# Performance work log

Measured on AMD Instinct MI355X. Metric: run time of the kernel, lower is better.

Reference implementation:

```python
import jax, jax.numpy as jnp
import numpy as np

WINDOWS = ((0, 4), (2, 6), (4, 8))
N_CLASSES = 64
EPS = 1e-12  # F.normalize eps


def setup_inputs() -> dict:
    key = jax.random.key(0)
    k1, k2 = jax.random.split(key)
    S, Q, T, D = 256, 4096, 8, 1024
    support_features = jax.random.normal(k1, (S, T, D), dtype=jnp.float32)
    target_features = jax.random.normal(k2, (Q, T, D), dtype=jnp.float32)
    support_labels = jnp.arange(S, dtype=jnp.int32) % N_CLASSES  # 4 shots per class, sorted-unique order
    logit_scale = jnp.array(0.0, dtype=jnp.float32)
    fusion_logits = jnp.zeros((3,), dtype=jnp.float32)
    return {
        'support_features': support_features,
        'target_features': target_features,
        'support_labels': support_labels,
        'logit_scale': logit_scale,
        'fusion_logits': fusion_logits,
    }


def _l2norm(x):
    n = jnp.sqrt(jnp.sum(x * x, axis=-1, keepdims=True))
    return x / jnp.maximum(n, EPS)


def _pairwise_dist(query_seq, support_seq):
    # query_seq: [Q, Tq, D], support_seq: [K, Ts, D] -> 1 - cosine sim [Q, K, Tq, Ts]
    sim = jnp.einsum('qtd,ksd->qkts', _l2norm(query_seq), _l2norm(support_seq))
    return 1.0 - sim


def _bi_mhm(dists):
    # dists: [Q, K, Tq, Ts]
    return dists.min(axis=3).sum(axis=2) + dists.min(axis=2).sum(axis=2)


def _segments(features):
    # features: [N, T, D] -> [N, n_windows, D] (mean over each window)
    return jnp.stack([features[:, s:e, :].mean(axis=1) for s, e in WINDOWS], axis=1)


def _prototypes(features, labels):
    # scatter-mean over class labels; features: [S, ...], labels: [S]
    sums = jax.ops.segment_sum(features, labels, num_segments=N_CLASSES)
    counts = jax.ops.segment_sum(jnp.ones((features.shape[0],), features.dtype), labels,
                                 num_segments=N_CLASSES)
    return sums / counts[:, None, None]


def reference(support_features, target_features, support_labels, logit_scale, fusion_logits):
    # global (frame-level) bidirectional min-sum chamfer distance to class prototypes
    support_proto = _prototypes(support_features, support_labels)          # [K, T, D]
    global_dist = _bi_mhm(_pairwise_dist(target_features, support_proto))  # [Q, K]

    # segment-level distances
    support_segments = _segments(support_features)                          # [S, 3, D]
    target_segments = _segments(target_features)                            # [Q, 3, D]
    support_seg_proto = _prototypes(support_segments, support_labels)       # [K, 3, D]
    seg_dist = _pairwise_dist(target_segments, support_seg_proto)           # [Q, K, 3, 3]
    seg_q2s = seg_dist.min(axis=3).sum(axis=2)
    seg_s2q = seg_dist.min(axis=2).sum(axis=2)

    fusion = jax.nn.softmax(fusion_logits)
    fused = (fusion[0] * global_dist + fusion[1] * seg_s2q + fusion[2] * seg_q2s)
    fused = fused * jnp.exp(logit_scale)
    return (-fused, -global_dist, -seg_s2q, -seg_q2s)
```

## Files before the change

### kernel.cpp

```cpp
#include <hip/hip_runtime.h>
#include <stdint.h>

typedef unsigned short u16;
typedef short short8 __attribute__((ext_vector_type(8)));
typedef float floatx4 __attribute__((ext_vector_type(4)));

#define KDIM 1024
#define QN   4096
#define KCLS 64
#define QK   (QN * KCLS)

#define DPP_XOR1 0xB1
#define DPP_XOR2 0x4E
#define DPP_HMIR 0x141
#define SWZ_XOR6  0x181F
#define SWZ_XOR16 0x401F

template <int CTRL>
__device__ __forceinline__ float dppf(float x) {
  int r = __builtin_amdgcn_mov_dpp(__builtin_bit_cast(int, x), CTRL, 0xF, 0xF, true);
  return __builtin_bit_cast(float, r);
}
template <int OFF>
__device__ __forceinline__ float swzf(float x) {
  int r = __builtin_amdgcn_ds_swizzle(__builtin_bit_cast(int, x), OFF);
  return __builtin_bit_cast(float, r);
}
__device__ __forceinline__ float max8(float x) {
  x = fmaxf(x, dppf<DPP_XOR1>(x));
  x = fmaxf(x, dppf<DPP_XOR2>(x));
  x = fmaxf(x, dppf<DPP_HMIR>(x));
  return x;
}
__device__ __forceinline__ float sum8(float x) {
  x += dppf<DPP_XOR1>(x);
  x += dppf<DPP_XOR2>(x);
  x += dppf<DPP_HMIR>(x);
  return x;
}


__device__ __forceinline__ u16 f2bf(float x) {
  union { float f; uint32_t u; } un; un.f = x;
  uint32_t u = un.u;
  u += 0x7FFFu + ((u >> 16) & 1u);
  return (u16)(u >> 16);
}

struct alignas(16) F4 { float x, y, z, w; };
struct alignas(8)  U16x4 { u16 a, b, c, d; };

__device__ __forceinline__ float dot4(const F4& a, const F4& b) {
  return a.x*b.x + a.y*b.y + a.z*b.z + a.w*b.w;
}

__device__ __forceinline__ void reduce11(float (&ss)[11], float (&tot)[11],
                                         float (*sb)[12], int lane, int wave) {
  #pragma unroll
  for (int v = 0; v < 11; ++v) {
    float x = ss[v];
    #pragma unroll
    for (int m = 1; m < 64; m <<= 1) x += __shfl_xor(x, m);
    ss[v] = x;
  }
  if (lane == 0) {
    #pragma unroll
    for (int v = 0; v < 11; ++v) sb[wave][v] = ss[v];
  }
  __syncthreads();
  #pragma unroll
  for (int v = 0; v < 11; ++v)
    tot[v] = sb[0][v] + sb[1][v] + sb[2][v] + sb[3][v];
}

__device__ __forceinline__ float inv_norm(float ss) {
  return 1.0f / fmaxf(sqrtf(ss), 1e-12f);
}

__global__ __launch_bounds__(256) void prep_all(const float* __restrict__ T,
                                                const float* __restrict__ S,
                                                u16* __restrict__ Ag,
                                                u16* __restrict__ Bg,
                                                float* __restrict__ invnT,
                                                float* __restrict__ invnTw,
                                                float* __restrict__ invnS,
                                                float* __restrict__ invnSw) {
  __shared__ float sb[4][12];
  const int b = blockIdx.x, tid = threadIdx.x;
  const int lane = tid & 63, wave = tid >> 6;

  if (b < QN) {
    const int q = b;
    F4 x[8];
    #pragma unroll
    for (int t = 0; t < 8; ++t)
      x[t] = *(const F4*)(T + (size_t)(q*8 + t)*1024 + tid*4);

    float ss[11], tot[11];
    #pragma unroll
    for (int t = 0; t < 8; ++t) ss[t] = dot4(x[t], x[t]);
    #pragma unroll
    for (int w = 0; w < 3; ++w) {
      F4 y;
      y.x = (x[2*w].x + x[2*w+1].x + x[2*w+2].x + x[2*w+3].x) * 0.25f;
      y.y = (x[2*w].y + x[2*w+1].y + x[2*w+2].y + x[2*w+3].y) * 0.25f;
      y.z = (x[2*w].z + x[2*w+1].z + x[2*w+2].z + x[2*w+3].z) * 0.25f;
      y.w = (x[2*w].w + x[2*w+1].w + x[2*w+2].w + x[2*w+3].w) * 0.25f;
      ss[8+w] = dot4(y, y);
    }
    reduce11(ss, tot, sb, lane, wave);

    #pragma unroll
    for (int t = 0; t < 8; ++t) {
      U16x4 o; o.a = f2bf(x[t].x); o.b = f2bf(x[t].y);
      o.c = f2bf(x[t].z); o.d = f2bf(x[t].w);
      *(U16x4*)(Ag + (size_t)(q*8 + t)*1024 + tid*4) = o;
    }
    if (tid < 8)       invnT [q*8 + tid]     = inv_norm(tot[tid]);
    else if (tid < 11) invnTw[q*4 + tid - 8] = inv_norm(tot[tid]);
  } else {
    const int k = b - QN;
    F4 p[8];
    #pragma unroll
    for (int t = 0; t < 8; ++t) { p[t].x = 0.f; p[t].y = 0.f; p[t].z = 0.f; p[t].w = 0.f; }
    #pragma unroll
    for (int s = 0; s < 4; ++s)
      #pragma unroll
      for (int t = 0; t < 8; ++t) {
        const F4 v = *(const F4*)(S + (size_t)(((s*64 + k)*8 + t))*1024 + tid*4);
        p[t].x += v.x; p[t].y += v.y; p[t].z += v.z; p[t].w += v.w;
      }
    float ss[11], tot[11];
    #pragma unroll
    for (int t = 0; t < 8; ++t) ss[t] = dot4(p[t], p[t]) * 0.0625f;
    #pragma unroll
    for (int w = 0; w < 3; ++w) {
      F4 y;
      y.x = (p[2*w].x + p[2*w+1].x + p[2*w+2].x + p[2*w+3].x) * 0.0625f;
      y.y = (p[2*w].y + p[2*w+1].y + p[2*w+2].y + p[2*w+3].y) * 0.0625f;
      y.z = (p[2*w].z + p[2*w+1].z + p[2*w+2].z + p[2*w+3].z) * 0.0625f;
      y.w = (p[2*w].w + p[2*w+1].w + p[2*w+2].w + p[2*w+3].w) * 0.0625f;
      ss[8+w] = dot4(y, y);
    }
    reduce11(ss, tot, sb, lane, wave);

    #pragma unroll
    for (int t = 0; t < 8; ++t) {
      U16x4 o; o.a = f2bf(p[t].x*0.25f); o.b = f2bf(p[t].y*0.25f);
      o.c = f2bf(p[t].z*0.25f); o.d = f2bf(p[t].w*0.25f);
      *(U16x4*)(Bg + (size_t)(k*8 + t)*1024 + tid*4) = o;
    }
    if (tid < 8)       invnS [k*8 + tid]     = inv_norm(tot[tid]);
    else if (tid < 11) invnSw[k*4 + tid - 8] = inv_norm(tot[tid]) * 0.0625f;
  }
}


__device__ __forceinline__ void load_lds16(const u16* g, u16* l) {
  __builtin_amdgcn_global_load_lds((__attribute__((address_space(1))) void*)(g),
                                   (__attribute__((address_space(3))) void*)(l),
                                   16, 0, 0);
}

__global__ __launch_bounds__(256) void gemm_all(const u16* __restrict__ A,
                                                const u16* __restrict__ B,
                                                const float* __restrict__ invnT,
                                                const float* __restrict__ invnTw,
                                                const float* __restrict__ invnS,
                                                const float* __restrict__ invnSw,
                                                float* __restrict__ outF,
                                                float* __restrict__ outG,
                                                float* __restrict__ outS2Q,
                                                float* __restrict__ outQ2S,
                                                const float* __restrict__ fl,
                                                const float* __restrict__ ls) {
  __shared__ __align__(16) u16 At[128 * 128];
  __shared__ __align__(16) u16 Bt[128 * 128];

  const int tid  = threadIdx.x;
  const int lane = tid & 63;
  const int wave = tid >> 6;
  const int wm = wave >> 1, wn = wave & 1;
  const int rowA0 = blockIdx.x * 128;
  const int rowB0 = blockIdx.y * 128;

  floatx4 acc[4][4] = {};

  const int srow = lane >> 4;
  const int sl   = lane & 15;

  for (int kb = 0; kb < KDIM; kb += 128) {
    __syncthreads();
    #pragma unroll
    for (int it = 0; it < 8; ++it) {
      const int c   = wave * 8 + it;
      const int row = c * 4 + srow;
      const int scol = ((sl ^ (row & 7)) * 8);
      load_lds16(A + (size_t)(rowA0 + row) * KDIM + kb + scol, &At[c * 512]);
      load_lds16(B + (size_t)(rowB0 + row) * KDIM + kb + scol, &Bt[c * 512]);
    }
    __syncthreads();
    const int q4 = lane >> 4;
    #pragma unroll
    for (int kk = 0; kk < 4; ++kk) {
      const int kc0 = kk * 4 + q4;
      short8 af[4], bf[4];
      #pragma unroll
      for (int i = 0; i < 4; ++i) {
        const int row = wm*64 + i*16 + (lane & 15);
        af[i] = *(const short8*)&At[row*128 + ((kc0 ^ (row & 7)) * 8)];
        const int col = wn*64 + i*16 + (lane & 15);
        bf[i] = *(const short8*)&Bt[col*128 + ((kc0 ^ (col & 7)) * 8)];
      }
      #pragma unroll
      for (int i = 0; i < 4; ++i)
        #pragma unroll
        for (int j = 0; j < 4; ++j)
          acc[i][j] = __builtin_amdgcn_mfma_f32_16x16x32_bf16(af[i], bf[j], acc[i][j], 0, 0, 0);
    }
  }

  const int sIdx = lane & 7;
  const int b3 = (lane >> 3) & 1;
  const int b4 = (lane >> 4) & 1;
  const int b5 = lane >> 5;
  const int qL = blockIdx.x * 16 + wm * 8;
  const int kL = blockIdx.y * 16 + wn * 8;

  float invT[4][4], invTw3[4][3], invS[4], invSw3[4][3];
  #pragma unroll
  for (int i = 0; i < 4; ++i) {
    const int q = qL + i*2 + b5;
    #pragma unroll
    for (int r = 0; r < 4; ++r) invT[i][r] = invnT[q*8 + b4*4 + r];
    #pragma unroll
    for (int w = 0; w < 3; ++w) invTw3[i][w] = invnTw[q*4 + w];
  }
  #pragma unroll
  for (int j = 0; j < 4; ++j) {
    const int k = kL + j*2 + b3;
    invS[j] = invnS[k*8 + sIdx];
    #pragma unroll
    for (int v = 0; v < 3; ++v) invSw3[j][v] = invnSw[k*4 + v];
  }

  const float f0 = fl[0], f1 = fl[1], f2 = fl[2];
  const float mx = fmaxf(f0, fmaxf(f1, f2));
  const float e0 = __expf(f0 - mx), e1 = __expf(f1 - mx), e2 = __expf(f2 - mx);
  const float sc = __expf(ls[0]) / (e0 + e1 + e2);

  const int vA = (sIdx < 4) ? 0 : 2;
  const bool v1ok = (sIdx >= 2) && (sIdx <= 5);

  #pragma unroll
  for (int i = 0; i < 4; ++i) {
    #pragma unroll
    for (int j = 0; j < 4; ++j) {
      const floatx4 c = acc[i][j];

      float sim[4];
      #pragma unroll
      for (int r = 0; r < 4; ++r) sim[r] = c[r] * invT[i][r] * invS[j];
      float rs = 0.f;
      #pragma unroll
      for (int r = 0; r < 4; ++r) rs += max8(sim[r]);
      rs += swzf<SWZ_XOR16>(rs);
      float cm = fmaxf(fmaxf(sim[0], sim[1]), fmaxf(sim[2], sim[3]));
      cm = fmaxf(cm, swzf<SWZ_XOR16>(cm));
      const float cs = sum8(cm);
      const float g = rs + cs - 16.0f;

      float wA[4], wB[4];
      #pragma unroll
      for (int r = 0; r < 4; ++r) {
        const float p2 = c[r] + dppf<DPP_XOR1>(c[r]);
        wA[r] = p2 + dppf<DPP_XOR2>(p2);
        wB[r] = p2 + swzf<SWZ_XOR6>(p2);
      }
      float twA[3], twB[3];
      {
        const float aAll = wA[0] + wA[1] + wA[2] + wA[3];
        const float aOth = swzf<SWZ_XOR16>(aAll);
        twA[0] = b4 ? aOth : aAll;
        twA[2] = b4 ? aAll : aOth;
        const float aH = b4 ? (wA[0] + wA[1]) : (wA[2] + wA[3]);
        twA[1] = aH + swzf<SWZ_XOR16>(aH);
        const float bAll = wB[0] + wB[1] + wB[2] + wB[3];
        const float bOth = swzf<SWZ_XOR16>(bAll);
        twB[0] = b4 ? bOth : bAll;
        twB[2] = b4 ? bAll : bOth;
        const float bH = b4 ? (wB[0] + wB[1]) : (wB[2] + wB[3]);
        twB[1] = bH + swzf<SWZ_XOR16>(bH);
      }
      float pA[3], pB[3];
      #pragma unroll
      for (int w = 0; w < 3; ++w) {
        pA[w] = twA[w] * invTw3[i][w] * invSw3[j][vA];
        pB[w] = twB[w] * invTw3[i][w] * invSw3[j][1];
      }
      float q2s = 0.f;
      #pragma unroll
      for (int w = 0; w < 3; ++w)
        q2s += max8(v1ok ? fmaxf(pA[w], pB[w]) : pA[w]);
      const float mwA = fmaxf(fmaxf(pA[0], pA[1]), pA[2]);
      const float mwB = fmaxf(fmaxf(pB[0], pB[1]), pB[2]);
      float contrib = ((sIdx == 0) | (sIdx == 4)) ? mwA : 0.f;
      if (sIdx == 2) contrib += mwB;
      const float s2q = sum8(contrib);

      if ((lane & 23) == 0) {
        const int q = qL + i*2 + b5;
        const int k = kL + j*2 + b3;
        const size_t idx = (size_t)q * KCLS + k;
        const float o1 = g;
        const float o2 = s2q - 3.0f;
        const float o3 = q2s - 3.0f;
        outG[idx]   = o1;
        outS2Q[idx] = o2;
        outQ2S[idx] = o3;
        outF[idx]   = sc * (e0 * o1 + e1 * o2 + e2 * o3);
      }
    }
  }
}


extern "C" void kernel_launch(void* const* d_in, const int* in_sizes, int n_in,
                              void* d_out, int out_size, void* d_ws, size_t ws_size,
                              hipStream_t stream) {
  (void)in_sizes; (void)n_in; (void)out_size; (void)ws_size;
  const float* S  = (const float*)d_in[0];
  const float* T  = (const float*)d_in[1];
  const float* ls = (const float*)d_in[3];
  const float* fl = (const float*)d_in[4];

  float* outF   = (float*)d_out;
  float* outG   = outF + QK;
  float* outS2Q = outF + 2 * (size_t)QK;
  float* outQ2S = outF + 3 * (size_t)QK;

  u16*   Ag     = (u16*)d_ws;
  u16*   Bg     = Ag + (size_t)32768 * 1024;
  float* invnT  = (float*)(Bg + (size_t)512 * 1024);
  float* invnTw = invnT + 32768;
  float* invnS  = invnTw + 16384;
  float* invnSw = invnS + 512;

  prep_all<<<QN + KCLS, 256, 0, stream>>>(T, S, Ag, Bg, invnT, invnTw, invnS, invnSw);

  gemm_all<<<dim3(256, 4), 256, 0, stream>>>(Ag, Bg, invnT, invnTw, invnS, invnSw,
                                             outF, outG, outS2Q, outQ2S, fl, ls);
}
```

Before: 268.3 us.

## Rewrite GEMM as 256x256 tile with double-buffered pipelined LDS staging

```diff
diff --git a/kernel.cpp b/kernel.cpp
--- a/kernel.cpp
+++ b/kernel.cpp
@@ -9,6 +9,7 @@
 #define QN   4096
 #define KCLS 64
 #define QK   (QN * KCLS)
+#define NKT  16
 
 #define DPP_XOR1 0xB1
 #define DPP_XOR2 0x4E
@@ -162,74 +163,160 @@
                                    16, 0, 0);
 }
 
-__global__ __launch_bounds__(256) void gemm_all(const u16* __restrict__ A,
-                                                const u16* __restrict__ B,
-                                                const float* __restrict__ invnT,
-                                                const float* __restrict__ invnTw,
-                                                const float* __restrict__ invnS,
-                                                const float* __restrict__ invnSw,
-                                                float* __restrict__ outF,
-                                                float* __restrict__ outG,
-                                                float* __restrict__ outS2Q,
-                                                float* __restrict__ outQ2S,
-                                                const float* __restrict__ fl,
-                                                const float* __restrict__ ls) {
-  __shared__ __align__(16) u16 At[128 * 128];
-  __shared__ __align__(16) u16 Bt[128 * 128];
+__device__ __forceinline__ void stage_half(const u16* __restrict__ A,
+                                           const u16* __restrict__ B,
+                                           u16* At_, u16* Bt_, int h,
+                                           int rowA0, int rowB0, int wave, int lane) {
+  const int tau = h >> 2, eta = h & 3;
+  const int kb = tau * 64;
+  const int half = eta & 1;
+  const int srow = lane >> 3, sl = lane & 7;
+  const int scol = (sl ^ srow) * 8;
+  const int region = (tau & 1) * 2 + half;
+  const int gr0 = ((eta < 2) ? rowA0 : rowB0) + half * 128;
+  const u16* gsrc = (eta < 2) ? A : B;
+  u16* ldst = (eta < 2) ? At_ : Bt_;
+  #pragma unroll
+  for (int r = 0; r < 2; ++r) {
+    const int c = r * 8 + wave;
+    const int row = c * 8 + srow;
+    load_lds16(gsrc + (size_t)(gr0 + row) * KDIM + kb + scol,
+               ldst + region * 8192 + c * 512);
+  }
+}
+
+__device__ __forceinline__ void ld_a(short8 (&dst)[4][2], const u16* At_,
+                                     int region, int lane, int i0) {
+  const int m = lane & 15, g = lane >> 4, r7 = lane & 7;
+  const u16* base = At_ + region * 8192;
+  #pragma unroll
+  for (int i = 0; i < 4; ++i)
+    #pragma unroll
+    for (int s = 0; s < 2; ++s) {
+      const int kc = s * 4 + g;
+      dst[i][s] = *(const short8*)&base[(i0 + i) * 1024 + m * 64 + ((kc ^ r7) * 8)];
+    }
+}
+
+__device__ __forceinline__ void ld_b(short8 (&dst)[2][2], const u16* Bt_,
+                                     int region, int colb, int lane, int j0) {
+  const int m = lane & 15, g = lane >> 4, r7 = lane & 7;
+  const u16* base = Bt_ + region * 8192;
+  #pragma unroll
+  for (int j = 0; j < 2; ++j)
+    #pragma unroll
+    for (int s = 0; s < 2; ++s) {
+      const int kc = s * 4 + g;
+      dst[j][s] = *(const short8*)&base[(colb + (j0 + j) * 16 + m) * 64 + ((kc ^ r7) * 8)];
+    }
+}
+
+#define SB()    __builtin_amdgcn_s_barrier()
+#define SCHED() __builtin_amdgcn_sched_barrier(0)
+#define MFMA16(AF, BF, I0, J0)                                                  \
+  do {                                                                          \
+    __builtin_amdgcn_s_setprio(1);                                              \
+    _Pragma("unroll") for (int i_ = 0; i_ < 4; ++i_)                            \
+      _Pragma("unroll") for (int j_ = 0; j_ < 2; ++j_)                          \
+        _Pragma("unroll") for (int s_ = 0; s_ < 2; ++s_)                        \
+          acc[(I0)+i_][(J0)+j_] = __builtin_amdgcn_mfma_f32_16x16x32_bf16(      \
+              AF[i_][s_], BF[j_][s_], acc[(I0)+i_][(J0)+j_], 0, 0, 0);          \
+    __builtin_amdgcn_s_setprio(0);                                              \
+  } while (0)
+
+__global__ __launch_bounds__(512, 2) void gemm_all(const u16* __restrict__ A,
+                                                   const u16* __restrict__ B,
+                                                   const float* __restrict__ invnT,
+                                                   const float* __restrict__ invnTw,
+                                                   const float* __restrict__ invnS,
+                                                   const float* __restrict__ invnSw,
+                                                   float* __restrict__ outF,
+                                                   float* __restrict__ outG,
+                                                   float* __restrict__ outS2Q,
+                                                   float* __restrict__ outQ2S,
+                                                   const float* __restrict__ fl,
+                                                   const float* __restrict__ ls) {
+  __shared__ __align__(16) u16 At[4 * 128 * 64];
+  __shared__ __align__(16) u16 Bt[4 * 128 * 64];
 
   const int tid  = threadIdx.x;
   const int lane = tid & 63;
   const int wave = tid >> 6;
-  const int wm = wave >> 1, wn = wave & 1;
-  const int rowA0 = blockIdx.x * 128;
-  const int rowB0 = blockIdx.y * 128;
-
-  floatx4 acc[4][4] = {};
-
-  const int srow = lane >> 4;
-  const int sl   = lane & 15;
-
-  for (int kb = 0; kb < KDIM; kb += 128) {
-    __syncthreads();
-    #pragma unroll
-    for (int it = 0; it < 8; ++it) {
-      const int c   = wave * 8 + it;
-      const int row = c * 4 + srow;
-      const int scol = ((sl ^ (row & 7)) * 8);
-      load_lds16(A + (size_t)(rowA0 + row) * KDIM + kb + scol, &At[c * 512]);
-      load_lds16(B + (size_t)(rowB0 + row) * KDIM + kb + scol, &Bt[c * 512]);
-    }
-    __syncthreads();
-    const int q4 = lane >> 4;
-    #pragma unroll
-    for (int kk = 0; kk < 4; ++kk) {
-      const int kc0 = kk * 4 + q4;
-      short8 af[4], bf[4];
-      #pragma unroll
-      for (int i = 0; i < 4; ++i) {
-        const int row = wm*64 + i*16 + (lane & 15);
-        af[i] = *(const short8*)&At[row*128 + ((kc0 ^ (row & 7)) * 8)];
-        const int col = wn*64 + i*16 + (lane & 15);
-        bf[i] = *(const short8*)&Bt[col*128 + ((kc0 ^ (col & 7)) * 8)];
-      }
-      #pragma unroll
-      for (int i = 0; i < 4; ++i)
-        #pragma unroll
-        for (int j = 0; j < 4; ++j)
-          acc[i][j] = __builtin_amdgcn_mfma_f32_16x16x32_bf16(af[i], bf[j], acc[i][j], 0, 0, 0);
-    }
+  const int wm = wave >> 2;
+  const int wn = wave & 3;
+  const int rowA0 = blockIdx.x * 256;
+  const int rowB0 = blockIdx.y * 256;
+  const int colb = (wn & 1) * 64;
+
+  floatx4 acc[8][4] = {};
+  short8 a0[4][2], a1[4][2], b0[2][2], b1[2][2];
+
+  #pragma unroll
+  for (int h = 0; h < 6; ++h)
+    stage_half(A, B, At, Bt, h, rowA0, rowB0, wave, lane);
+
+  #pragma unroll 1
+  for (int t = 0; t < NKT - 1; ++t) {
+    const int buf = t & 1;
+    const int ra = buf * 2 + wm;
+    const int rb = buf * 2 + (wn >> 1);
+    stage_half(A, B, At, Bt, 4*t + 6, rowA0, rowB0, wave, lane);
+    SCHED();
+    asm volatile("s_waitcnt vmcnt(6)");
+    SCHED();
+    SB(); SCHED();
+    ld_a(a0, At, ra, lane, 0);
+    ld_b(b0, Bt, rb, colb, lane, 0);
+    MFMA16(a0, b0, 0, 0);
+    SB(); SCHED();
+    stage_half(A, B, At, Bt, 4*t + 7, rowA0, rowB0, wave, lane);
+    SCHED();
+    SB(); SCHED();
+    ld_a(a1, At, ra, lane, 4);
+    MFMA16(a1, b0, 4, 0);
+    SB(); SCHED();
+    if (4*t + 8 < 4*NKT)
+      stage_half(A, B, At, Bt, 4*t + 8, rowA0, rowB0, wave, lane);
+    SCHED();
+    SB(); SCHED();
+    ld_b(b1, Bt, rb, colb, lane, 2);
+    MFMA16(a0, b1, 0, 2);
+    SB(); SCHED();
+    if (4*t + 9 < 4*NKT)
+      stage_half(A, B, At, Bt, 4*t + 9, rowA0, rowB0, wave, lane);
+    SCHED();
+    SB(); SCHED();
+    MFMA16(a1, b1, 4, 2);
+    SB(); SCHED();
+  }
+  {
+    const int ra = 2 + wm;
+    const int rb = 2 + (wn >> 1);
+    asm volatile("s_waitcnt vmcnt(0)");
+    SCHED();
+    SB(); SCHED();
+    ld_a(a0, At, ra, lane, 0);
+    ld_b(b0, Bt, rb, colb, lane, 0);
+    MFMA16(a0, b0, 0, 0);
+    SB(); SCHED();
+    ld_a(a1, At, ra, lane, 4);
+    MFMA16(a1, b0, 4, 0);
+    SB(); SCHED();
+    ld_b(b1, Bt, rb, colb, lane, 2);
+    MFMA16(a0, b1, 0, 2);
+    MFMA16(a1, b1, 4, 2);
   }
 
   const int sIdx = lane & 7;
   const int b3 = (lane >> 3) & 1;
   const int b4 = (lane >> 4) & 1;
   const int b5 = lane >> 5;
-  const int qL = blockIdx.x * 16 + wm * 8;
-  const int kL = blockIdx.y * 16 + wn * 8;
-
-  float invT[4][4], invTw3[4][3], invS[4], invSw3[4][3];
-  #pragma unroll
-  for (int i = 0; i < 4; ++i) {
+  const int qL = blockIdx.x * 32 + wm * 16;
+  const int kL = blockIdx.y * 32 + wn * 8;
+
+  float invT[8][4], invTw3[8][3], invS[4], invSw3[4][3];
+  #pragma unroll
+  for (int i = 0; i < 8; ++i) {
     const int q = qL + i*2 + b5;
     #pragma unroll
     for (int r = 0; r < 4; ++r) invT[i][r] = invnT[q*8 + b4*4 + r];
@@ -253,7 +340,7 @@
   const bool v1ok = (sIdx >= 2) && (sIdx <= 5);
 
   #pragma unroll
-  for (int i = 0; i < 4; ++i) {
+  for (int i = 0; i < 8; ++i) {
     #pragma unroll
     for (int j = 0; j < 4; ++j) {
       const floatx4 c = acc[i][j];
@@ -348,6 +435,6 @@
 
   prep_all<<<QN + KCLS, 256, 0, stream>>>(T, S, Ag, Bg, invnT, invnTw, invnS, invnSw);
 
-  gemm_all<<<dim3(256, 4), 256, 0, stream>>>(Ag, Bg, invnT, invnTw, invnS, invnSw,
+  gemm_all<<<dim3(128, 2), 512, 0, stream>>>(Ag, Bg, invnT, invnTw, invnS, invnSw,
                                              outF, outG, outS2Q, outQ2S, fl, ls);
 }
```

After: 266.0 us. No clear change (-0.8%).

## Fuse query bf16 conversion and norms into GEMM with double-buffered B staging

Applied to the files above, without the earlier changes.

```diff
diff --git a/kernel.cpp b/kernel.cpp
--- a/kernel.cpp
+++ b/kernel.cpp
@@ -9,6 +9,7 @@
 #define QN   4096
 #define KCLS 64
 #define QK   (QN * KCLS)
+#define NKT  16
 
 #define DPP_XOR1 0xB1
 #define DPP_XOR2 0x4E
@@ -54,107 +55,12 @@
   return a.x*b.x + a.y*b.y + a.z*b.z + a.w*b.w;
 }
 
-__device__ __forceinline__ void reduce11(float (&ss)[11], float (&tot)[11],
-                                         float (*sb)[12], int lane, int wave) {
-  #pragma unroll
-  for (int v = 0; v < 11; ++v) {
-    float x = ss[v];
-    #pragma unroll
-    for (int m = 1; m < 64; m <<= 1) x += __shfl_xor(x, m);
-    ss[v] = x;
-  }
-  if (lane == 0) {
-    #pragma unroll
-    for (int v = 0; v < 11; ++v) sb[wave][v] = ss[v];
-  }
-  __syncthreads();
-  #pragma unroll
-  for (int v = 0; v < 11; ++v)
-    tot[v] = sb[0][v] + sb[1][v] + sb[2][v] + sb[3][v];
-}
-
 __device__ __forceinline__ float inv_norm(float ss) {
   return 1.0f / fmaxf(sqrtf(ss), 1e-12f);
 }
 
-__global__ __launch_bounds__(256) void prep_all(const float* __restrict__ T,
-                                                const float* __restrict__ S,
-                                                u16* __restrict__ Ag,
-                                                u16* __restrict__ Bg,
-                                                float* __restrict__ invnT,
-                                                float* __restrict__ invnTw,
-                                                float* __restrict__ invnS,
-                                                float* __restrict__ invnSw) {
-  __shared__ float sb[4][12];
-  const int b = blockIdx.x, tid = threadIdx.x;
-  const int lane = tid & 63, wave = tid >> 6;
-
-  if (b < QN) {
-    const int q = b;
-    F4 x[8];
-    #pragma unroll
-    for (int t = 0; t < 8; ++t)
-      x[t] = *(const F4*)(T + (size_t)(q*8 + t)*1024 + tid*4);
-
-    float ss[11], tot[11];
-    #pragma unroll
-    for (int t = 0; t < 8; ++t) ss[t] = dot4(x[t], x[t]);
-    #pragma unroll
-    for (int w = 0; w < 3; ++w) {
-      F4 y;
-      y.x = (x[2*w].x + x[2*w+1].x + x[2*w+2].x + x[2*w+3].x) * 0.25f;
-      y.y = (x[2*w].y + x[2*w+1].y + x[2*w+2].y + x[2*w+3].y) * 0.25f;
-      y.z = (x[2*w].z + x[2*w+1].z + x[2*w+2].z + x[2*w+3].z) * 0.25f;
-      y.w = (x[2*w].w + x[2*w+1].w + x[2*w+2].w + x[2*w+3].w) * 0.25f;
-      ss[8+w] = dot4(y, y);
-    }
-    reduce11(ss, tot, sb, lane, wave);
-
-    #pragma unroll
-    for (int t = 0; t < 8; ++t) {
-      U16x4 o; o.a = f2bf(x[t].x); o.b = f2bf(x[t].y);
-      o.c = f2bf(x[t].z); o.d = f2bf(x[t].w);
-      *(U16x4*)(Ag + (size_t)(q*8 + t)*1024 + tid*4) = o;
-    }
-    if (tid < 8)       invnT [q*8 + tid]     = inv_norm(tot[tid]);
-    else if (tid < 11) invnTw[q*4 + tid - 8] = inv_norm(tot[tid]);
-  } else {
-    const int k = b - QN;
-    F4 p[8];
-    #pragma unroll
-    for (int t = 0; t < 8; ++t) { p[t].x = 0.f; p[t].y = 0.f; p[t].z = 0.f; p[t].w = 0.f; }
-    #pragma unroll
-    for (int s = 0; s < 4; ++s)
-      #pragma unroll
-      for (int t = 0; t < 8; ++t) {
-        const F4 v = *(const F4*)(S + (size_t)(((s*64 + k)*8 + t))*1024 + tid*4);
-        p[t].x += v.x; p[t].y += v.y; p[t].z += v.z; p[t].w += v.w;
-      }
-    float ss[11], tot[11];
-    #pragma unroll
-    for (int t = 0; t < 8; ++t) ss[t] = dot4(p[t], p[t]) * 0.0625f;
-    #pragma unroll
-    for (int w = 0; w < 3; ++w) {
-      F4 y;
-      y.x = (p[2*w].x + p[2*w+1].x + p[2*w+2].x + p[2*w+3].x) * 0.0625f;
-      y.y = (p[2*w].y + p[2*w+1].y + p[2*w+2].y + p[2*w+3].y) * 0.0625f;
-      y.z = (p[2*w].z + p[2*w+1].z + p[2*w+2].z + p[2*w+3].z) * 0.0625f;
-      y.w = (p[2*w].w + p[2*w+1].w + p[2*w+2].w + p[2*w+3].w) * 0.0625f;
-      ss[8+w] = dot4(y, y);
-    }
-    reduce11(ss, tot, sb, lane, wave);
-
-    #pragma unroll
-    for (int t = 0; t < 8; ++t) {
-      U16x4 o; o.a = f2bf(p[t].x*0.25f); o.b = f2bf(p[t].y*0.25f);
-      o.c = f2bf(p[t].z*0.25f); o.d = f2bf(p[t].w*0.25f);
-      *(U16x4*)(Bg + (size_t)(k*8 + t)*1024 + tid*4) = o;
-    }
-    if (tid < 8)       invnS [k*8 + tid]     = inv_norm(tot[tid]);
-    else if (tid < 11) invnSw[k*4 + tid - 8] = inv_norm(tot[tid]) * 0.0625f;
-  }
-}
-
+#define SB()    __builtin_amdgcn_s_barrier()
+#define SCHED() __builtin_amdgcn_sched_barrier(0)
 
 __device__ __forceinline__ void load_lds16(const u16* g, u16* l) {
   __builtin_amdgcn_global_load_lds((__attribute__((address_space(1))) void*)(g),
@@ -162,86 +68,220 @@
                                    16, 0, 0);
 }
 
-__global__ __launch_bounds__(256) void gemm_all(const u16* __restrict__ A,
-                                                const u16* __restrict__ B,
-                                                const float* __restrict__ invnT,
-                                                const float* __restrict__ invnTw,
-                                                const float* __restrict__ invnS,
-                                                const float* __restrict__ invnSw,
-                                                float* __restrict__ outF,
-                                                float* __restrict__ outG,
-                                                float* __restrict__ outS2Q,
-                                                float* __restrict__ outQ2S,
-                                                const float* __restrict__ fl,
-                                                const float* __restrict__ ls) {
-  __shared__ __align__(16) u16 At[128 * 128];
-  __shared__ __align__(16) u16 Bt[128 * 128];
+__global__ __launch_bounds__(256) void prep_B(const float* __restrict__ S,
+                                              u16* __restrict__ Bg,
+                                              float* __restrict__ invnS,
+                                              float* __restrict__ invnSw) {
+  __shared__ float sb[4][12];
+  const int k = blockIdx.x, tid = threadIdx.x;
+  const int lane = tid & 63, wave = tid >> 6;
+
+  F4 p[8];
+  #pragma unroll
+  for (int t = 0; t < 8; ++t) { p[t].x = 0.f; p[t].y = 0.f; p[t].z = 0.f; p[t].w = 0.f; }
+  #pragma unroll
+  for (int s = 0; s < 4; ++s)
+    #pragma unroll
+    for (int t = 0; t < 8; ++t) {
+      const F4 v = *(const F4*)(S + (size_t)(((s*64 + k)*8 + t))*1024 + tid*4);
+      p[t].x += v.x; p[t].y += v.y; p[t].z += v.z; p[t].w += v.w;
+    }
+  float ss[11], tot[11];
+  #pragma unroll
+  for (int t = 0; t < 8; ++t) ss[t] = dot4(p[t], p[t]) * 0.0625f;
+  #pragma unroll
+  for (int w = 0; w < 3; ++w) {
+    F4 y;
+    y.x = (p[2*w].x + p[2*w+1].x + p[2*w+2].x + p[2*w+3].x) * 0.0625f;
+    y.y = (p[2*w].y + p[2*w+1].y + p[2*w+2].y + p[2*w+3].y) * 0.0625f;
+    y.z = (p[2*w].z + p[2*w+1].z + p[2*w+2].z + p[2*w+3].z) * 0.0625f;
+    y.w = (p[2*w].w + p[2*w+1].w + p[2*w+2].w + p[2*w+3].w) * 0.0625f;
+    ss[8+w] = dot4(y, y);
+  }
+  #pragma unroll
+  for (int v = 0; v < 11; ++v) {
+    float x = ss[v];
+    #pragma unroll
+    for (int m = 1; m < 64; m <<= 1) x += __shfl_xor(x, m);
+    ss[v] = x;
+  }
+  if (lane == 0) {
+    #pragma unroll
+    for (int v = 0; v < 11; ++v) sb[wave][v] = ss[v];
+  }
+  __syncthreads();
+  #pragma unroll
+  for (int v = 0; v < 11; ++v)
+    tot[v] = sb[0][v] + sb[1][v] + sb[2][v] + sb[3][v];
+
+  #pragma unroll
+  for (int t = 0; t < 8; ++t) {
+    U16x4 o; o.a = f2bf(p[t].x*0.25f); o.b = f2bf(p[t].y*0.25f);
+    o.c = f2bf(p[t].z*0.25f); o.d = f2bf(p[t].w*0.25f);
+    *(U16x4*)(Bg + (size_t)(k*8 + t)*1024 + tid*4) = o;
+  }
+  if (tid < 8)       invnS [k*8 + tid]     = inv_norm(tot[tid]);
+  else if (tid < 11) invnSw[k*4 + tid - 8] = inv_norm(tot[tid]) * 0.0625f;
+}
+
+__global__ __launch_bounds__(512, 1) void fused_all(const float* __restrict__ T,
+                                                    const u16* __restrict__ Bg,
+                                                    const float* __restrict__ invnS,
+                                                    const float* __restrict__ invnSw,
+                                                    float* __restrict__ outF,
+                                                    float* __restrict__ outG,
+                                                    float* __restrict__ outS2Q,
+                                                    float* __restrict__ outQ2S,
+                                                    const float* __restrict__ fl,
+                                                    const float* __restrict__ ls) {
+  __shared__ __align__(16) u16 At[128 * 64];
+  __shared__ __align__(16) u16 Bt[2][512 * 64];
 
   const int tid  = threadIdx.x;
   const int lane = tid & 63;
   const int wave = tid >> 6;
-  const int wm = wave >> 1, wn = wave & 1;
-  const int rowA0 = blockIdx.x * 128;
-  const int rowB0 = blockIdx.y * 128;
-
-  floatx4 acc[4][4] = {};
-
-  const int srow = lane >> 4;
-  const int sl   = lane & 15;
-
-  for (int kb = 0; kb < KDIM; kb += 128) {
-    __syncthreads();
-    #pragma unroll
-    for (int it = 0; it < 8; ++it) {
-      const int c   = wave * 8 + it;
-      const int row = c * 4 + srow;
-      const int scol = ((sl ^ (row & 7)) * 8);
-      load_lds16(A + (size_t)(rowA0 + row) * KDIM + kb + scol, &At[c * 512]);
-      load_lds16(B + (size_t)(rowB0 + row) * KDIM + kb + scol, &Bt[c * 512]);
-    }
-    __syncthreads();
-    const int q4 = lane >> 4;
-    #pragma unroll
-    for (int kk = 0; kk < 4; ++kk) {
-      const int kc0 = kk * 4 + q4;
-      short8 af[4], bf[4];
-      #pragma unroll
-      for (int i = 0; i < 4; ++i) {
-        const int row = wm*64 + i*16 + (lane & 15);
-        af[i] = *(const short8*)&At[row*128 + ((kc0 ^ (row & 7)) * 8)];
-        const int col = wn*64 + i*16 + (lane & 15);
-        bf[i] = *(const short8*)&Bt[col*128 + ((kc0 ^ (col & 7)) * 8)];
-      }
-      #pragma unroll
-      for (int i = 0; i < 4; ++i)
+  const int wm = wave >> 1;
+  const int wn = wave & 1;
+  const int bx = blockIdx.x;
+
+  const int srow8 = lane >> 3, sl8 = lane & 7;
+  const int scolB = (sl8 ^ srow8) * 8;
+
+  const float* Tw = T + ((size_t)bx * 128 + wave * 16) * KDIM + lane;
+
+  floatx4 acc[2][16] = {};
+  float ssRow[16] = {};
+  float ssW0[3] = {}, ssW1[3] = {};
+  float x[16];
+  short8 af[2][2];
+
+  const int m16 = lane & 15, g4 = lane >> 4, r7 = lane & 7;
+
+  auto stageB = [&](int t) {
+    u16* dst = &Bt[t & 1][0];
+    #pragma unroll
+    for (int r = 0; r < 8; ++r) {
+      const int c = wave * 8 + r;
+      const int row = c * 8 + srow8;
+      load_lds16(Bg + (size_t)row * KDIM + t * 64 + scolB, dst + c * 512);
+    }
+  };
+  auto loadX = [&](int t) {
+    #pragma unroll
+    for (int r = 0; r < 16; ++r) x[r] = Tw[(size_t)r * KDIM + t * 64];
+  };
+  auto cvtWriteNorm = [&]() {
+    #pragma unroll
+    for (int r = 0; r < 16; ++r) {
+      const int row = wave * 16 + r;
+      At[row * 64 + (((lane >> 3) ^ (r & 7)) * 8) + (lane & 7)] = f2bf(x[r]);
+      ssRow[r] += x[r] * x[r];
+    }
+    #pragma unroll
+    for (int w = 0; w < 3; ++w) {
+      const float a0 = (x[2*w] + x[2*w+1] + x[2*w+2] + x[2*w+3]) * 0.25f;
+      ssW0[w] += a0 * a0;
+      const float a1 = (x[8+2*w] + x[8+2*w+1] + x[8+2*w+2] + x[8+2*w+3]) * 0.25f;
+      ssW1[w] += a1 * a1;
+    }
+  };
+  auto ldA = [&]() {
+    #pragma unroll
+    for (int i = 0; i < 2; ++i)
+      #pragma unroll
+      for (int s = 0; s < 2; ++s) {
+        const int row = wm * 32 + i * 16 + m16;
+        af[i][s] = *(const short8*)&At[row * 64 + (((s * 4 + g4) ^ r7) * 8)];
+      }
+  };
+  auto mfmaPhase = [&](int buf) {
+    const u16* Bb = &Bt[buf][0];
+    #pragma unroll
+    for (int jc = 0; jc < 8; ++jc) {
+      short8 bf[2][2];
+      #pragma unroll
+      for (int j2 = 0; j2 < 2; ++j2)
         #pragma unroll
-        for (int j = 0; j < 4; ++j)
-          acc[i][j] = __builtin_amdgcn_mfma_f32_16x16x32_bf16(af[i], bf[j], acc[i][j], 0, 0, 0);
-    }
-  }
+        for (int s = 0; s < 2; ++s) {
+          const int rowb = wn * 256 + (jc * 2 + j2) * 16 + m16;
+          bf[j2][s] = *(const short8*)&Bb[rowb * 64 + (((s * 4 + g4) ^ r7) * 8)];
+        }
+      #pragma unroll
+      for (int i = 0; i < 2; ++i)
+        #pragma unroll
+        for (int j2 = 0; j2 < 2; ++j2)
+          #pragma unroll
+          for (int s = 0; s < 2; ++s)
+            acc[i][jc * 2 + j2] = __builtin_amdgcn_mfma_f32_16x16x32_bf16(
+                af[i][s], bf[j2][s], acc[i][jc * 2 + j2], 0, 0, 0);
+    }
+  };
+
+  loadX(0);
+  stageB(0);
+  cvtWriteNorm();
+  SCHED();
+  asm volatile("s_waitcnt vmcnt(0) lgkmcnt(0)");
+  SCHED();
+  SB(); SCHED();
+
+  #pragma unroll 1
+  for (int t = 0; t < NKT; ++t) {
+    ldA();
+    if (t < NKT - 1) { loadX(t + 1); stageB(t + 1); }
+    SCHED();
+    asm volatile("s_waitcnt lgkmcnt(0)");
+    SCHED();
+    SB(); SCHED();
+    mfmaPhase(t & 1);
+    if (t < NKT - 1) cvtWriteNorm();
+    SCHED();
+    asm volatile("s_waitcnt vmcnt(0) lgkmcnt(0)");
+    SCHED();
+    SB(); SCHED();
+  }
+
+  float* invT_l  = (float*)At;
+  float* invTw_l = invT_l + 128;
+  #pragma unroll
+  for (int r = 0; r < 16; ++r) {
+    float v = ssRow[r];
+    #pragma unroll
+    for (int mk = 1; mk < 64; mk <<= 1) v += __shfl_xor(v, mk);
+    if (lane == 0) invT_l[wave * 16 + r] = inv_norm(v);
+  }
+  #pragma unroll
+  for (int w = 0; w < 3; ++w) {
+    float v0 = ssW0[w], v1 = ssW1[w];
+    #pragma unroll
+    for (int mk = 1; mk < 64; mk <<= 1) { v0 += __shfl_xor(v0, mk); v1 += __shfl_xor(v1, mk); }
+    if (lane == 0) {
+      invTw_l[(wave * 2 + 0) * 3 + w] = inv_norm(v0);
+      invTw_l[(wave * 2 + 1) * 3 + w] = inv_norm(v1);
+    }
+  }
+  __syncthreads();
 
   const int sIdx = lane & 7;
   const int b3 = (lane >> 3) & 1;
   const int b4 = (lane >> 4) & 1;
   const int b5 = lane >> 5;
-  const int qL = blockIdx.x * 16 + wm * 8;
-  const int kL = blockIdx.y * 16 + wn * 8;
-
-  float invT[4][4], invTw3[4][3], invS[4], invSw3[4][3];
-  #pragma unroll
-  for (int i = 0; i < 4; ++i) {
-    const int q = qL + i*2 + b5;
-    #pragma unroll
-    for (int r = 0; r < 4; ++r) invT[i][r] = invnT[q*8 + b4*4 + r];
-    #pragma unroll
-    for (int w = 0; w < 3; ++w) invTw3[i][w] = invnTw[q*4 + w];
-  }
-  #pragma unroll
-  for (int j = 0; j < 4; ++j) {
-    const int k = kL + j*2 + b3;
-    invS[j] = invnS[k*8 + sIdx];
-    #pragma unroll
-    for (int v = 0; v < 3; ++v) invSw3[j][v] = invnSw[k*4 + v];
+
+  float invT[2][4], invTw3[2][3], invS[16], invSw3[16][3];
+  #pragma unroll
+  for (int i = 0; i < 2; ++i) {
+    const int ql = wm * 4 + i * 2 + b5;
+    #pragma unroll
+    for (int r = 0; r < 4; ++r) invT[i][r] = invT_l[ql * 8 + b4 * 4 + r];
+    #pragma unroll
+    for (int w = 0; w < 3; ++w) invTw3[i][w] = invTw_l[ql * 3 + w];
+  }
+  #pragma unroll
+  for (int j = 0; j < 16; ++j) {
+    const int k = wn * 32 + j * 2 + b3;
+    invS[j] = invnS[k * 8 + sIdx];
+    #pragma unroll
+    for (int v = 0; v < 3; ++v) invSw3[j][v] = invnSw[k * 4 + v];
   }
 
   const float f0 = fl[0], f1 = fl[1], f2 = fl[2];
@@ -253,9 +293,9 @@
   const bool v1ok = (sIdx >= 2) && (sIdx <= 5);
 
   #pragma unroll
-  for (int i = 0; i < 4; ++i) {
-    #pragma unroll
-    for (int j = 0; j < 4; ++j) {
+  for (int i = 0; i < 2; ++i) {
+    #pragma unroll
+    for (int j = 0; j < 16; ++j) {
       const floatx4 c = acc[i][j];
 
       float sim[4];
@@ -309,8 +349,8 @@
       const float s2q = sum8(contrib);
 
       if ((lane & 23) == 0) {
-        const int q = qL + i*2 + b5;
-        const int k = kL + j*2 + b3;
+        const int q = bx * 16 + wm * 4 + i * 2 + b5;
+        const int k = wn * 32 + j * 2 + b3;
         const size_t idx = (size_t)q * KCLS + k;
         const float o1 = g;
         const float o2 = s2q - 3.0f;
@@ -339,15 +379,12 @@
   float* outS2Q = outF + 2 * (size_t)QK;
   float* outQ2S = outF + 3 * (size_t)QK;
 
-  u16*   Ag     = (u16*)d_ws;
-  u16*   Bg     = Ag + (size_t)32768 * 1024;
-  float* invnT  = (float*)(Bg + (size_t)512 * 1024);
-  float* invnTw = invnT + 32768;
-  float* invnS  = invnTw + 16384;
+  u16*   Bg     = (u16*)d_ws;
+  float* invnS  = (float*)(Bg + (size_t)512 * 1024);
   float* invnSw = invnS + 512;
 
-  prep_all<<<QN + KCLS, 256, 0, stream>>>(T, S, Ag, Bg, invnT, invnTw, invnS, invnSw);
-
-  gemm_all<<<dim3(256, 4), 256, 0, stream>>>(Ag, Bg, invnT, invnTw, invnS, invnSw,
-                                             outF, outG, outS2Q, outQ2S, fl, ls);
-}
+  prep_B<<<KCLS, 256, 0, stream>>>(S, Bg, invnS, invnSw);
+
+  fused_all<<<256, 512, 0, stream>>>(T, Bg, invnS, invnSw,
+                                     outF, outG, outS2Q, outQ2S, fl, ls);
+}
```

Result: no change. 265.3 us, median of 2 (-1.1%).
